# Optimization experiments

Hardware: AMD Instinct MI355X
Metric: run time of the kernel (lower is better)

## Reference

```python
import jax, jax.numpy as jnp
import numpy as np

N_NODES = 100000
N_EDGES = 1600000
NODE_DIM = 3
EDGE_DIM = 32
HIDDEN = 128
OUT_DIM = 3
N_GRAPHS = 64


def _lin(key, fan_in, fan_out):
    k1, k2 = jax.random.split(key)
    s = 1.0 / np.sqrt(fan_in)
    W = jax.random.uniform(k1, (fan_in, fan_out), minval=-s, maxval=s, dtype=jnp.float32)
    b = jax.random.uniform(k2, (fan_out,), minval=-s, maxval=s, dtype=jnp.float32)
    return W, b


def setup_inputs() -> dict:
    key = jax.random.key(0)
    ks = jax.random.split(key, 16)
    x = jax.random.normal(ks[0], (N_NODES, NODE_DIM), dtype=jnp.float32)
    edge_index = jax.random.randint(ks[1], (2, N_EDGES), 0, N_NODES, dtype=jnp.int32)
    edge_attr = jax.random.normal(ks[2], (N_EDGES, EDGE_DIM), dtype=jnp.float32)
    batch = jnp.sort(jax.random.randint(ks[3], (N_NODES,), 0, N_GRAPHS, dtype=jnp.int32))
    # conv1: CGConv at channels=NODE_DIM, in = 2*NODE_DIM + EDGE_DIM
    Wf1, bf1 = _lin(ks[4], 2 * NODE_DIM + EDGE_DIM, NODE_DIM)
    Ws1, bs1 = _lin(ks[5], 2 * NODE_DIM + EDGE_DIM, NODE_DIM)
    Wp, bp = _lin(ks[6], NODE_DIM, HIDDEN)
    # two hidden CGConvs at channels=HIDDEN
    Wf2, bf2 = _lin(ks[7], 2 * HIDDEN + EDGE_DIM, HIDDEN)
    Ws2, bs2 = _lin(ks[8], 2 * HIDDEN + EDGE_DIM, HIDDEN)
    Wf3, bf3 = _lin(ks[9], 2 * HIDDEN + EDGE_DIM, HIDDEN)
    Ws3, bs3 = _lin(ks[10], 2 * HIDDEN + EDGE_DIM, HIDDEN)
    W1, b1 = _lin(ks[11], HIDDEN, HIDDEN)
    W2, b2 = _lin(ks[12], HIDDEN, OUT_DIM)
    return dict(x=x, edge_index=edge_index, edge_attr=edge_attr, batch=batch,
                Wf1=Wf1, bf1=bf1, Ws1=Ws1, bs1=bs1, Wp=Wp, bp=bp,
                Wf2=Wf2, bf2=bf2, Ws2=Ws2, bs2=bs2,
                Wf3=Wf3, bf3=bf3, Ws3=Ws3, bs3=bs3,
                W1=W1, b1=b1, W2=W2, b2=b2)


def _cgconv(x, src, dst, edge_attr, Wf, bf, Ws, bs):
    # z = [x_i (target), x_j (source), e_ij]; message = sigmoid(lin_f(z)) * softplus(lin_s(z))
    z = jnp.concatenate([x[dst], x[src], edge_attr], axis=-1)  # [E, 2C+F]
    m = jax.nn.sigmoid(z @ Wf + bf) * jax.nn.softplus(z @ Ws + bs)  # [E, C]
    agg = jax.ops.segment_sum(m, dst, num_segments=x.shape[0])
    return x + agg


def reference(x, edge_index, edge_attr, batch,
              Wf1, bf1, Ws1, bs1, Wp, bp,
              Wf2, bf2, Ws2, bs2, Wf3, bf3, Ws3, bs3,
              W1, b1, W2, b2):
    src, dst = edge_index[0], edge_index[1]
    h = _cgconv(x, src, dst, edge_attr, Wf1, bf1, Ws1, bs1)
    h = jax.nn.relu(h @ Wp + bp)
    h = jax.nn.relu(_cgconv(h, src, dst, edge_attr, Wf2, bf2, Ws2, bs2))
    h = jax.nn.relu(_cgconv(h, src, dst, edge_attr, Wf3, bf3, Ws3, bs3))
    # global mean pool over graphs
    sums = jax.ops.segment_sum(h, batch, num_segments=N_GRAPHS)
    counts = jax.ops.segment_sum(jnp.ones((h.shape[0],), h.dtype), batch, num_segments=N_GRAPHS)
    pooled = sums / jnp.maximum(counts, 1.0)[:, None]
    g = jax.nn.relu(pooled @ W1 + b1)
    return g @ W2 + b2
```

## Files before the change

kernel.cpp:

```cpp
#include <hip/hip_runtime.h>
#include <hip/hip_bf16.h>


#define N_NODES 100000
#define N_EDGES 1600000
#define HID 128
#define SCAN_BLOCKS 391

typedef unsigned int uint;
typedef short bf16x8 __attribute__((ext_vector_type(8)));
typedef float f32x4 __attribute__((ext_vector_type(4)));

__device__ inline float bflo(uint u) { return __uint_as_float(u << 16); }
__device__ inline float bfhi(uint u) { return __uint_as_float(u & 0xffff0000u); }
__device__ inline uint pack_bf16_2(float a, float b) {
  uint ua = __float_as_uint(a), ub = __float_as_uint(b);
  ua = (ua + 0x7fffu + ((ua >> 16) & 1u)) >> 16;
  ub = (ub + 0x7fffu + ((ub >> 16) & 1u)) >> 16;
  return ua | (ub << 16);
}
__device__ inline float sigmoidf_(float x) {
  return __builtin_amdgcn_rcpf(1.f + __expf(-x));
}
__device__ inline float softplusf_(float x) {
  return fmaxf(x, 0.f) + __logf(1.f + __expf(-fabsf(x)));
}

__global__ __launch_bounds__(256) void hist_k(const int* __restrict__ ei,
                                              int* __restrict__ deg) {
  int e = blockIdx.x * 256 + threadIdx.x;
  if (e >= N_EDGES) return;
  atomicAdd(&deg[ei[N_EDGES + e]], 1);
}

__global__ __launch_bounds__(256) void scan1_k(const int* __restrict__ deg,
                                               int* __restrict__ rowptr,
                                               int* __restrict__ bsums) {
  __shared__ int s[256];
  int i = blockIdx.x * 256 + threadIdx.x;
  int v = (i < N_NODES) ? deg[i] : 0;
  s[threadIdx.x] = v;
  __syncthreads();
  for (int off = 1; off < 256; off <<= 1) {
    int t = (threadIdx.x >= off) ? s[threadIdx.x - off] : 0;
    __syncthreads();
    s[threadIdx.x] += t;
    __syncthreads();
  }
  if (i < N_NODES) rowptr[i] = s[threadIdx.x] - v;
  if (threadIdx.x == 255) bsums[blockIdx.x] = s[255];
}

__global__ __launch_bounds__(512) void scan2_k(int* __restrict__ bsums) {
  __shared__ int s[512];
  int t = threadIdx.x;
  int v = (t < SCAN_BLOCKS) ? bsums[t] : 0;
  s[t] = v;
  __syncthreads();
  for (int off = 1; off < 512; off <<= 1) {
    int x = (t >= off) ? s[t - off] : 0;
    __syncthreads();
    s[t] += x;
    __syncthreads();
  }
  if (t < SCAN_BLOCKS) bsums[t] = s[t] - v;
}

__global__ __launch_bounds__(256) void scan3_k(int* __restrict__ rowptr,
                                               const int* __restrict__ bsums,
                                               int* __restrict__ cur) {
  int i = blockIdx.x * 256 + threadIdx.x;
  if (i < N_NODES) {
    int r = rowptr[i] + bsums[blockIdx.x];
    rowptr[i] = r;
    cur[i] = r;
  }
  if (i == 0) rowptr[N_NODES] = N_EDGES;
}

__global__ __launch_bounds__(256) void scatter_k(const int* __restrict__ ei,
                                                 int* __restrict__ cur,
                                                 uint4* __restrict__ csr) {
  int e = blockIdx.x * 256 + threadIdx.x;
  if (e >= N_EDGES) return;
  int d = ei[N_EDGES + e];
  int pos = atomicAdd(&cur[d], 1);
  csr[pos] = make_uint4((uint)ei[e], (uint)e, (uint)d, 0u);
}

__global__ __launch_bounds__(256) void conv1_edge(
    const float* __restrict__ x, const int* __restrict__ ei,
    const float* __restrict__ ea,
    const float* __restrict__ Wf, const float* __restrict__ bf,
    const float* __restrict__ Ws, const float* __restrict__ bs,
    float* __restrict__ agg1) {
  int e = blockIdx.x * 256 + threadIdx.x;
  if (e >= N_EDGES) return;
  int src = ei[e], dst = ei[N_EDGES + e];
  float z[38];
#pragma unroll
  for (int k = 0; k < 3; ++k) z[k] = x[dst * 3 + k];
#pragma unroll
  for (int k = 0; k < 3; ++k) z[3 + k] = x[src * 3 + k];
  const float4* er4 = (const float4*)(ea + (long long)e * 32);
#pragma unroll
  for (int k = 0; k < 8; ++k) {
    float4 v = er4[k];
    z[6 + 4 * k + 0] = v.x;
    z[6 + 4 * k + 1] = v.y;
    z[6 + 4 * k + 2] = v.z;
    z[6 + 4 * k + 3] = v.w;
  }
#pragma unroll
  for (int c = 0; c < 3; ++c) {
    float f = bf[c], s = bs[c];
#pragma unroll
    for (int k = 0; k < 38; ++k) {
      f = fmaf(z[k], Wf[k * 3 + c], f);
      s = fmaf(z[k], Ws[k * 3 + c], s);
    }
    atomicAdd(&agg1[dst * 3 + c], sigmoidf_(f) * softplusf_(s));
  }
}

__global__ __launch_bounds__(256) void proj_kernel(
    const float* __restrict__ x, const float* __restrict__ agg1,
    const float* __restrict__ Wp, const float* __restrict__ bp,
    float* __restrict__ h) {
  long long i = (long long)blockIdx.x * 256 + threadIdx.x;
  if (i >= (long long)N_NODES * HID) return;
  int n = (int)(i >> 7), j = (int)(i & 127);
  float v0 = x[n * 3 + 0] + agg1[n * 3 + 0];
  float v1 = x[n * 3 + 1] + agg1[n * 3 + 1];
  float v2 = x[n * 3 + 2] + agg1[n * 3 + 2];
  float acc = bp[j];
  acc = fmaf(v0, Wp[0 * HID + j], acc);
  acc = fmaf(v1, Wp[1 * HID + j], acc);
  acc = fmaf(v2, Wp[2 * HID + j], acc);
  h[i] = fmaxf(acc, 0.f);
}

#define BM 64
#define BK 32

__global__ __launch_bounds__(256) void node_gemm2(
    const float* __restrict__ h, const float* __restrict__ Wf,
    const float* __restrict__ Ws, const float* __restrict__ bf,
    const float* __restrict__ bs, uint* __restrict__ Pb) {
  __shared__ float As[BK][BM + 4];
  __shared__ float BfS[BK][BM + 4];
  __shared__ float BsS[BK][BM + 4];
  int jblk = blockIdx.x;
  int part = jblk >> 1;
  int colbase = (jblk & 1) * 64;
  int rowoff = part * 128;
  int m0 = blockIdx.y * BM;
  int tid = threadIdx.x, tx = tid & 15, ty = tid >> 4;
  float accF[4][4] = {}, accS[4][4] = {};
  for (int k0 = 0; k0 < 128; k0 += BK) {
#pragma unroll
    for (int i = 0; i < 2; ++i) {
      int f = tid + i * 256;
      int r = f >> 3, c4 = (f & 7) * 4;
      float4 v = {0.f, 0.f, 0.f, 0.f};
      int row = m0 + r;
      if (row < N_NODES)
        v = *(const float4*)&h[(long long)row * 128 + k0 + c4];
      As[c4 + 0][r] = v.x; As[c4 + 1][r] = v.y;
      As[c4 + 2][r] = v.z; As[c4 + 3][r] = v.w;
    }
#pragma unroll
    for (int i = 0; i < 2; ++i) {
      int f = tid + i * 256;
      int r = f >> 4, c4 = (f & 15) * 4;
      *(float4*)&BfS[r][c4] =
          *(const float4*)&Wf[(long long)(k0 + r + rowoff) * 128 + colbase + c4];
      *(float4*)&BsS[r][c4] =
          *(const float4*)&Ws[(long long)(k0 + r + rowoff) * 128 + colbase + c4];
    }
    __syncthreads();
#pragma unroll
    for (int k = 0; k < BK; ++k) {
      float4 a = *(const float4*)&As[k][ty * 4];
      float4 bF = *(const float4*)&BfS[k][tx * 4];
      float4 bS = *(const float4*)&BsS[k][tx * 4];
      float av[4] = {a.x, a.y, a.z, a.w};
      float bFv[4] = {bF.x, bF.y, bF.z, bF.w};
      float bSv[4] = {bS.x, bS.y, bS.z, bS.w};
#pragma unroll
      for (int i = 0; i < 4; ++i)
#pragma unroll
        for (int j = 0; j < 4; ++j) {
          accF[i][j] = fmaf(av[i], bFv[j], accF[i][j]);
          accS[i][j] = fmaf(av[i], bSv[j], accS[i][j]);
        }
    }
    __syncthreads();
  }
  float fbias[4] = {0.f, 0.f, 0.f, 0.f}, sbias[4] = {0.f, 0.f, 0.f, 0.f};
  if (part == 0) {
#pragma unroll
    for (int j = 0; j < 4; ++j) {
      fbias[j] = bf[colbase + tx * 4 + j];
      sbias[j] = bs[colbase + tx * 4 + j];
    }
  }
#pragma unroll
  for (int i = 0; i < 4; ++i) {
    int row = m0 + ty * 4 + i;
    if (row < N_NODES) {
      uint4 o;
      o.x = pack_bf16_2(accF[i][0] + fbias[0], accS[i][0] + sbias[0]);
      o.y = pack_bf16_2(accF[i][1] + fbias[1], accS[i][1] + sbias[1]);
      o.z = pack_bf16_2(accF[i][2] + fbias[2], accS[i][2] + sbias[2]);
      o.w = pack_bf16_2(accF[i][3] + fbias[3], accS[i][3] + sbias[3]);
      *(uint4*)&Pb[(long long)row * 256 + part * 128 + colbase + tx * 4] = o;
    }
  }
}

__global__ __launch_bounds__(256) void w_prep(const float* __restrict__ Wf,
                                              const float* __restrict__ Ws,
                                              uint* __restrict__ Btg) {
  int t = threadIdx.x;
  const float* W = (t < 128) ? Wf : Ws;
  int c = t & 127;
#pragma unroll
  for (int kk = 0; kk < 16; ++kk) {
    float a = W[(256 + 2 * kk) * 128 + c];
    float b = W[(256 + 2 * kk + 1) * 128 + c];
    Btg[t * 16 + kk] = pack_bf16_2(a, b);
  }
}

#define EMSG_EB 64
#define LSTR 20
__global__ __launch_bounds__(256, 4) void edge_msg(
    const uint* __restrict__ Pb, const float* __restrict__ ea,
    const uint* __restrict__ Btg, const uint4* __restrict__ csr,
    float* __restrict__ h) {
  __shared__ uint Alds[EMSG_EB * LSTR];
  __shared__ uint Blds[256 * LSTR];
  int tid = threadIdx.x;
  int j0 = blockIdx.x * EMSG_EB;
  {
    const uint4* s4 = (const uint4*)(Btg + tid * 16);
    uint4 v0 = s4[0], v1 = s4[1], v2 = s4[2], v3 = s4[3];
    uint* d = &Blds[tid * LSTR];
    *(uint4*)(d + 0) = v0; *(uint4*)(d + 4) = v1;
    *(uint4*)(d + 8) = v2; *(uint4*)(d + 12) = v3;
  }
  {
    int r = tid >> 2, q = tid & 3;
    uint e = csr[j0 + r].y;
    const float4* er = (const float4*)(ea + (long long)e * 32 + q * 8);
    float4 a0 = er[0], a1 = er[1];
    uint4 pk;
    pk.x = pack_bf16_2(a0.x, a0.y);
    pk.y = pack_bf16_2(a0.z, a0.w);
    pk.z = pack_bf16_2(a1.x, a1.y);
    pk.w = pack_bf16_2(a1.z, a1.w);
    *(uint4*)&Alds[r * LSTR + q * 4] = pk;
  }
  __syncthreads();
  int wave = tid >> 6, lane = tid & 63;
  int c0w = wave * 32;
  int l15 = lane & 15, lq = lane >> 4;
  bf16x8 afr[4], bfr[4];
#pragma unroll
  for (int mt = 0; mt < 4; ++mt)
    afr[mt] = *(const bf16x8*)&Alds[(mt * 16 + l15) * LSTR + lq * 4];
  int chs0 = c0w + l15, chs1 = c0w + 16 + l15;
  bfr[0] = *(const bf16x8*)&Blds[chs0 * LSTR + lq * 4];
  bfr[1] = *(const bf16x8*)&Blds[chs1 * LSTR + lq * 4];
  bfr[2] = *(const bf16x8*)&Blds[(128 + chs0) * LSTR + lq * 4];
  bfr[3] = *(const bf16x8*)&Blds[(128 + chs1) * LSTR + lq * 4];
  f32x4 acc[4][4];
#pragma unroll
  for (int mt = 0; mt < 4; ++mt)
#pragma unroll
    for (int nt = 0; nt < 4; ++nt) {
      f32x4 z = {0.f, 0.f, 0.f, 0.f};
      acc[mt][nt] = __builtin_amdgcn_mfma_f32_16x16x32_bf16(afr[mt], bfr[nt], z, 0, 0, 0);
    }
#pragma unroll
  for (int mt = 0; mt < 4; ++mt) {
    int jb = j0 + mt * 16 + lq * 4;
    uint srcs[4], dsts[4];
#pragma unroll
    for (int reg = 0; reg < 4; ++reg) {
      uint4 cj = csr[jb + reg];
      srcs[reg] = cj.x;
      dsts[reg] = cj.z;
    }
#pragma unroll
    for (int cp = 0; cp < 2; ++cp) {
      int c = (cp ? chs1 : chs0);
      float mr[4];
#pragma unroll
      for (int reg = 0; reg < 4; ++reg) {
        uint gd = Pb[(long long)dsts[reg] * 256 + c];
        uint gs = Pb[(long long)srcs[reg] * 256 + 128 + c];
        float f = acc[mt][cp][reg] + bflo(gd) + bflo(gs);
        float s = acc[mt][2 + cp][reg] + bfhi(gd) + bfhi(gs);
        mr[reg] = sigmoidf_(f) * softplusf_(s);
      }
      float racc = mr[0];
#pragma unroll
      for (int reg = 1; reg < 4; ++reg) {
        if (dsts[reg] == dsts[reg - 1]) {
          racc += mr[reg];
        } else {
          atomicAdd(&h[(long long)dsts[reg - 1] * HID + c], racc);
          racc = mr[reg];
        }
      }
      atomicAdd(&h[(long long)dsts[3] * HID + c], racc);
    }
  }
}

__global__ __launch_bounds__(256) void relu_k(float* __restrict__ h) {
  const int total = N_NODES * HID / 4;
  for (int i = blockIdx.x * 256 + threadIdx.x; i < total; i += gridDim.x * 256) {
    float4 v = ((float4*)h)[i];
    v.x = fmaxf(v.x, 0.f); v.y = fmaxf(v.y, 0.f);
    v.z = fmaxf(v.z, 0.f); v.w = fmaxf(v.w, 0.f);
    ((float4*)h)[i] = v;
  }
}

#define POOL_NODES 128
__global__ __launch_bounds__(128) void pool2(
    const float* __restrict__ h, const int* __restrict__ batch,
    float* __restrict__ sums, float* __restrict__ cnts) {
  int n0 = blockIdx.x * POOL_NODES;
  if (n0 >= N_NODES) return;
  int t = threadIdx.x;
  int nEnd = n0 + POOL_NODES;
  if (nEnd > N_NODES) nEnd = N_NODES;
  float acc = 0.f;
  int bcur = batch[n0];
  int cnt = 0;
  for (int n = n0; n < nEnd; ++n) {
    int b = batch[n];
    if (b != bcur) {
      atomicAdd(&sums[bcur * HID + t], acc);
      if (t == 0) atomicAdd(&cnts[bcur], (float)cnt);
      acc = 0.f; cnt = 0; bcur = b;
    }
    acc += h[(long long)n * HID + t];
    ++cnt;
  }
  atomicAdd(&sums[bcur * HID + t], acc);
  if (t == 0) atomicAdd(&cnts[bcur], (float)cnt);
}

__global__ __launch_bounds__(128) void mlpA(
    const float* __restrict__ sums, const float* __restrict__ cnts,
    const float* __restrict__ W1, const float* __restrict__ b1,
    float* __restrict__ g) {
  __shared__ float pl[HID];
  int gr = blockIdx.x, j = threadIdx.x;
  float cnt = fmaxf(cnts[gr], 1.f);
  pl[j] = sums[gr * HID + j] / cnt;
  __syncthreads();
  float acc = b1[j];
#pragma unroll 8
  for (int k = 0; k < HID; ++k) acc = fmaf(pl[k], W1[k * HID + j], acc);
  g[gr * HID + j] = fmaxf(acc, 0.f);
}

__global__ __launch_bounds__(256) void mlpB(
    const float* __restrict__ g, const float* __restrict__ W2,
    const float* __restrict__ b2, float* __restrict__ out) {
  int t = threadIdx.x;
  if (t >= 64 * 3) return;
  int gr = t / 3, o = t % 3;
  float acc = b2[o];
#pragma unroll 8
  for (int k = 0; k < HID; ++k) acc = fmaf(g[gr * HID + k], W2[k * 3 + o], acc);
  out[t] = acc;
}

extern "C" void kernel_launch(void* const* d_in, const int* in_sizes, int n_in,
                              void* d_out, int out_size, void* d_ws, size_t ws_size,
                              hipStream_t stream) {
  const float* x   = (const float*)d_in[0];
  const int*   ei  = (const int*)d_in[1];
  const float* ea  = (const float*)d_in[2];
  const int*   bat = (const int*)d_in[3];
  const float* Wf1 = (const float*)d_in[4];
  const float* bf1 = (const float*)d_in[5];
  const float* Ws1 = (const float*)d_in[6];
  const float* bs1 = (const float*)d_in[7];
  const float* Wp  = (const float*)d_in[8];
  const float* bp  = (const float*)d_in[9];
  const float* Wf2 = (const float*)d_in[10];
  const float* bf2 = (const float*)d_in[11];
  const float* Ws2 = (const float*)d_in[12];
  const float* bs2 = (const float*)d_in[13];
  const float* Wf3 = (const float*)d_in[14];
  const float* bf3 = (const float*)d_in[15];
  const float* Ws3 = (const float*)d_in[16];
  const float* bs3 = (const float*)d_in[17];
  const float* W1  = (const float*)d_in[18];
  const float* b1  = (const float*)d_in[19];
  const float* W2  = (const float*)d_in[20];
  const float* b2  = (const float*)d_in[21];
  float* out = (float*)d_out;

  char* w = (char*)d_ws;
  size_t off = 0;
  auto alloc = [&](size_t bytes) {
    void* p = w + off;
    off += (bytes + 255) & ~(size_t)255;
    return p;
  };
  int*   deg    = (int*)alloc((size_t)N_NODES * 4);
  int*   rowptr = (int*)alloc((size_t)(N_NODES + 1) * 4);
  int*   cur    = (int*)alloc((size_t)N_NODES * 4);
  int*   bsums  = (int*)alloc((size_t)512 * 4);
  uint4* csr    = (uint4*)alloc((size_t)N_EDGES * 16);
  float* agg1   = (float*)alloc((size_t)N_NODES * 3 * 4);
  float* h      = (float*)alloc((size_t)N_NODES * HID * 4);
  uint*  Pb     = (uint*)alloc((size_t)N_NODES * 256 * 4);
  float* sums   = (float*)alloc((size_t)64 * HID * 4);
  float* cnts   = (float*)alloc((size_t)64 * 4);
  float* g      = (float*)alloc((size_t)64 * HID * 4);
  uint*  Btg    = (uint*)alloc((size_t)256 * 16 * 4);
  (void)ws_size;

  hipMemsetAsync(deg, 0, (size_t)N_NODES * 4, stream);
  hist_k<<<(N_EDGES + 255) / 256, 256, 0, stream>>>(ei, deg);
  scan1_k<<<SCAN_BLOCKS, 256, 0, stream>>>(deg, rowptr, bsums);
  scan2_k<<<1, 512, 0, stream>>>(bsums);
  scan3_k<<<SCAN_BLOCKS, 256, 0, stream>>>(rowptr, bsums, cur);
  scatter_k<<<(N_EDGES + 255) / 256, 256, 0, stream>>>(ei, cur, csr);

  hipMemsetAsync(agg1, 0, (size_t)N_NODES * 3 * 4, stream);
  conv1_edge<<<(N_EDGES + 255) / 256, 256, 0, stream>>>(x, ei, ea, Wf1, bf1, Ws1, bs1, agg1);
  proj_kernel<<<(N_NODES * HID + 255) / 256, 256, 0, stream>>>(x, agg1, Wp, bp, h);

  dim3 ngrid2(4, (N_NODES + BM - 1) / BM);
  int eblocks = N_EDGES / EMSG_EB;

  node_gemm2<<<ngrid2, 256, 0, stream>>>(h, Wf2, Ws2, bf2, bs2, Pb);
  w_prep<<<1, 256, 0, stream>>>(Wf2, Ws2, Btg);
  edge_msg<<<eblocks, 256, 0, stream>>>(Pb, ea, Btg, csr, h);
  relu_k<<<4096, 256, 0, stream>>>(h);

  node_gemm2<<<ngrid2, 256, 0, stream>>>(h, Wf3, Ws3, bf3, bs3, Pb);
  w_prep<<<1, 256, 0, stream>>>(Wf3, Ws3, Btg);
  edge_msg<<<eblocks, 256, 0, stream>>>(Pb, ea, Btg, csr, h);
  relu_k<<<4096, 256, 0, stream>>>(h);

  hipMemsetAsync(sums, 0, (size_t)(64 * HID + 64) * 4, stream);
  pool2<<<(N_NODES + POOL_NODES - 1) / POOL_NODES, POOL_NODES, 0, stream>>>(h, bat, sums, cnts);
  mlpA<<<64, 128, 0, stream>>>(sums, cnts, W1, b1, g);
  mlpB<<<1, 256, 0, stream>>>(g, W2, b2, out);
}
```

Measured before the change: 2.287 ms.

## Pre-pack edge attributes to bf16 in CSR order and aggregate per block in LDS

A new ea_pack kernel converts edge attributes to bf16 once, in CSR order, so both edge_msg launches read contiguous packed rows instead of gathering fp32 rows through the edge permutation. Inside edge_msg, destinations in each 64-edge tile are deduplicated with a ballot, and per-destination partial sums are accumulated with LDS atomics. Each block then flushes one global atomic per destination and channel, and nodes whose whole edge range falls inside the tile get a plain store with ReLU applied. The cost is an extra packing pass, 100 MB more workspace, and more LDS per block, which may reduce occupancy.

```diff
diff --git a/kernel.cpp b/kernel.cpp
--- a/kernel.cpp
+++ b/kernel.cpp
@@ -86,6 +86,23 @@
   int d = ei[N_EDGES + e];
   int pos = atomicAdd(&cur[d], 1);
   csr[pos] = make_uint4((uint)ei[e], (uint)e, (uint)d, 0u);
+}
+
+__global__ __launch_bounds__(256) void ea_pack(const float* __restrict__ ea,
+                                               const uint4* __restrict__ csr,
+                                               uint4* __restrict__ eab) {
+  long long t = (long long)blockIdx.x * 256 + threadIdx.x;
+  int p = (int)(t >> 2), q = (int)(t & 3);
+  if (p >= N_EDGES) return;
+  uint e = csr[p].y;
+  const float4* er = (const float4*)(ea + (long long)e * 32 + q * 8);
+  float4 a0 = er[0], a1 = er[1];
+  uint4 pk;
+  pk.x = pack_bf16_2(a0.x, a0.y);
+  pk.y = pack_bf16_2(a0.z, a0.w);
+  pk.z = pack_bf16_2(a1.x, a1.y);
+  pk.w = pack_bf16_2(a1.z, a1.w);
+  eab[(long long)p * 4 + q] = pk;
 }
 
 __global__ __launch_bounds__(256) void conv1_edge(
@@ -235,14 +252,24 @@
 
 #define EMSG_EB 64
 #define LSTR 20
+#define CAP 16
 __global__ __launch_bounds__(256, 4) void edge_msg(
-    const uint* __restrict__ Pb, const float* __restrict__ ea,
+    const uint* __restrict__ Pb, const uint4* __restrict__ eab,
     const uint* __restrict__ Btg, const uint4* __restrict__ csr,
-    float* __restrict__ h) {
+    const int* __restrict__ rowptr, float* __restrict__ h) {
   __shared__ uint Alds[EMSG_EB * LSTR];
   __shared__ uint Blds[256 * LSTR];
+  __shared__ float accL[CAP * 128];
+  __shared__ int dstL[64], srcL[64], liL[64];
+  __shared__ int dlist[CAP], compL[CAP];
+  __shared__ int nDistS;
   int tid = threadIdx.x;
   int j0 = blockIdx.x * EMSG_EB;
+  {
+    int r = tid >> 2, q = tid & 3;
+    uint4 v = eab[(long long)j0 * 4 + tid];
+    *(uint4*)&Alds[r * LSTR + q * 4] = v;
+  }
   {
     const uint4* s4 = (const uint4*)(Btg + tid * 16);
     uint4 v0 = s4[0], v1 = s4[1], v2 = s4[2], v3 = s4[3];
@@ -250,17 +277,25 @@
     *(uint4*)(d + 0) = v0; *(uint4*)(d + 4) = v1;
     *(uint4*)(d + 8) = v2; *(uint4*)(d + 12) = v3;
   }
-  {
-    int r = tid >> 2, q = tid & 3;
-    uint e = csr[j0 + r].y;
-    const float4* er = (const float4*)(ea + (long long)e * 32 + q * 8);
-    float4 a0 = er[0], a1 = er[1];
-    uint4 pk;
-    pk.x = pack_bf16_2(a0.x, a0.y);
-    pk.y = pack_bf16_2(a0.z, a0.w);
-    pk.z = pack_bf16_2(a1.x, a1.y);
-    pk.w = pack_bf16_2(a1.z, a1.w);
-    *(uint4*)&Alds[r * LSTR + q * 4] = pk;
+#pragma unroll
+  for (int i = 0; i < (CAP * 128) / 256; ++i) accL[tid + i * 256] = 0.f;
+  if (tid < 64) {
+    uint4 cj = csr[j0 + tid];
+    int d = (int)cj.z;
+    dstL[tid] = d;
+    srcL[tid] = (int)cj.x;
+    int dprev = __shfl_up(d, 1, 64);
+    bool flag = (tid == 0) || (d != dprev);
+    unsigned long long m = __ballot(flag);
+    unsigned long long pre = (tid == 63) ? ~0ull : ((1ull << (tid + 1)) - 1);
+    int li = __popcll(m & pre) - 1;
+    liL[tid] = li;
+    if (flag && li < CAP) {
+      dlist[li] = d;
+      int r0 = rowptr[d], r1 = rowptr[d + 1];
+      compL[li] = ((r0 == j0 + tid) && (r1 <= j0 + EMSG_EB)) ? 1 : 0;
+    }
+    if (tid == 0) nDistS = __popcll(m);
   }
   __syncthreads();
   int wave = tid >> 6, lane = tid & 63;
@@ -285,13 +320,12 @@
     }
 #pragma unroll
   for (int mt = 0; mt < 4; ++mt) {
-    int jb = j0 + mt * 16 + lq * 4;
-    uint srcs[4], dsts[4];
+    int o = mt * 16 + lq * 4;
+    int dsts[4], lis[4];
 #pragma unroll
     for (int reg = 0; reg < 4; ++reg) {
-      uint4 cj = csr[jb + reg];
-      srcs[reg] = cj.x;
-      dsts[reg] = cj.z;
+      dsts[reg] = dstL[o + reg];
+      lis[reg] = liL[o + reg];
     }
 #pragma unroll
     for (int cp = 0; cp < 2; ++cp) {
@@ -300,22 +334,39 @@
 #pragma unroll
       for (int reg = 0; reg < 4; ++reg) {
         uint gd = Pb[(long long)dsts[reg] * 256 + c];
-        uint gs = Pb[(long long)srcs[reg] * 256 + 128 + c];
+        uint gs = Pb[(long long)srcL[o + reg] * 256 + 128 + c];
         float f = acc[mt][cp][reg] + bflo(gd) + bflo(gs);
         float s = acc[mt][2 + cp][reg] + bfhi(gd) + bfhi(gs);
         mr[reg] = sigmoidf_(f) * softplusf_(s);
       }
       float racc = mr[0];
+      int cl = lis[0], cd = dsts[0];
 #pragma unroll
       for (int reg = 1; reg < 4; ++reg) {
-        if (dsts[reg] == dsts[reg - 1]) {
+        if (lis[reg] == cl) {
           racc += mr[reg];
         } else {
-          atomicAdd(&h[(long long)dsts[reg - 1] * HID + c], racc);
-          racc = mr[reg];
+          if (cl < CAP) atomicAdd(&accL[cl * 128 + c], racc);
+          else atomicAdd(&h[(long long)cd * HID + c], racc);
+          cl = lis[reg]; cd = dsts[reg]; racc = mr[reg];
         }
       }
-      atomicAdd(&h[(long long)dsts[3] * HID + c], racc);
+      if (cl < CAP) atomicAdd(&accL[cl * 128 + c], racc);
+      else atomicAdd(&h[(long long)cd * HID + c], racc);
+    }
+  }
+  __syncthreads();
+  int nD = nDistS;
+  if (nD > CAP) nD = CAP;
+  int c = tid & 127;
+  for (int li = tid >> 7; li < nD; li += 2) {
+    int d = dlist[li];
+    float v = accL[li * 128 + c];
+    float* hp = &h[(long long)d * HID + c];
+    if (compL[li]) {
+      *hp = fmaxf(*hp + v, 0.f);
+    } else {
+      atomicAdd(hp, v);
     }
   }
 }
@@ -425,6 +476,7 @@
   float* agg1   = (float*)alloc((size_t)N_NODES * 3 * 4);
   float* h      = (float*)alloc((size_t)N_NODES * HID * 4);
   uint*  Pb     = (uint*)alloc((size_t)N_NODES * 256 * 4);
+  uint4* eab    = (uint4*)alloc((size_t)N_EDGES * 64);
   float* sums   = (float*)alloc((size_t)64 * HID * 4);
   float* cnts   = (float*)alloc((size_t)64 * 4);
   float* g      = (float*)alloc((size_t)64 * HID * 4);
@@ -437,6 +489,7 @@
   scan2_k<<<1, 512, 0, stream>>>(bsums);
   scan3_k<<<SCAN_BLOCKS, 256, 0, stream>>>(rowptr, bsums, cur);
   scatter_k<<<(N_EDGES + 255) / 256, 256, 0, stream>>>(ei, cur, csr);
+  ea_pack<<<(N_EDGES * 4 + 255) / 256, 256, 0, stream>>>(ea, csr, eab);
 
   hipMemsetAsync(agg1, 0, (size_t)N_NODES * 3 * 4, stream);
   conv1_edge<<<(N_EDGES + 255) / 256, 256, 0, stream>>>(x, ei, ea, Wf1, bf1, Ws1, bs1, agg1);
@@ -447,12 +500,12 @@
 
   node_gemm2<<<ngrid2, 256, 0, stream>>>(h, Wf2, Ws2, bf2, bs2, Pb);
   w_prep<<<1, 256, 0, stream>>>(Wf2, Ws2, Btg);
-  edge_msg<<<eblocks, 256, 0, stream>>>(Pb, ea, Btg, csr, h);
+  edge_msg<<<eblocks, 256, 0, stream>>>(Pb, eab, Btg, csr, rowptr, h);
   relu_k<<<4096, 256, 0, stream>>>(h);
 
   node_gemm2<<<ngrid2, 256, 0, stream>>>(h, Wf3, Ws3, bf3, bs3, Pb);
   w_prep<<<1, 256, 0, stream>>>(Wf3, Ws3, Btg);
-  edge_msg<<<eblocks, 256, 0, stream>>>(Pb, ea, Btg, csr, h);
+  edge_msg<<<eblocks, 256, 0, stream>>>(Pb, eab, Btg, csr, rowptr, h);
   relu_k<<<4096, 256, 0, stream>>>(h);
 
   hipMemsetAsync(sums, 0, (size_t)(64 * HID + 64) * 4, stream);
```

After: 2.038 ms. 1.12x faster.
